# Performance work log

Hardware: AMD Instinct MI355X
Metric: run time of the kernel (lower is better)

Reference implementation:

```python
import jax, jax.numpy as jnp
import numpy as np
from jax import lax

NUM_HEADS = 4
NUM_GROUPS = 32
EPS = 1e-5


def group_norm(x, gamma, beta):
    # x: [b, c, t]
    b, c, t = x.shape
    xg = x.reshape(b, NUM_GROUPS, c // NUM_GROUPS, t)
    mu = jnp.mean(xg, axis=(2, 3), keepdims=True)
    var = jnp.var(xg, axis=(2, 3), keepdims=True)
    xg = (xg - mu) * lax.rsqrt(var + EPS)
    x = xg.reshape(b, c, t)
    return x * gamma[None, :, None] + beta[None, :, None]


def conv1d_same(x, w, b):
    # x: [b, c_in, t], w: [c_out, c_in, k] -> TF-style SAME padding, stride 1
    k = w.shape[-1]
    left = (k - 1) // 2
    right = (k - 1) - left
    y = lax.conv_general_dilated(x, w, window_strides=(1,),
                                 padding=[(left, right)],
                                 dimension_numbers=('NCH', 'OIH', 'NCH'))
    return y + b[None, :, None]


def qkv_attention(qkv):
    # qkv: [b*heads, 3*ch, t]
    ch = qkv.shape[1] // 3
    q, k, v = jnp.split(qkv, 3, axis=1)
    scale = float(ch) ** -0.25  # 1/sqrt(sqrt(ch)) applied to both q and k
    w = jnp.einsum('bct,bcs->bts', q * scale, k * scale)
    w = jax.nn.softmax(w.astype(jnp.float32), axis=-1).astype(qkv.dtype)
    return jnp.einsum('bts,bcs->bct', w, v)


def setup_inputs() -> dict:
    key = jax.random.key(0)
    ks = jax.random.split(key, 5)
    B, C, H, W = 4, 512, 64, 64
    x = jax.random.normal(ks[0], (B, C, H, W), dtype=jnp.float32)
    gn_gamma = jnp.ones((C,), dtype=jnp.float32)
    gn_beta = jnp.zeros((C,), dtype=jnp.float32)
    qkv_w = jax.random.normal(ks[1], (3 * C, C, C // 16), dtype=jnp.float32) * 0.02
    qkv_b = jax.random.normal(ks[2], (3 * C,), dtype=jnp.float32) * 0.02
    proj_w = jax.random.normal(ks[3], (C, C, 5), dtype=jnp.float32) * 0.02
    proj_b = jax.random.normal(ks[4], (C,), dtype=jnp.float32) * 0.02
    return {"x": x, "gn_gamma": gn_gamma, "gn_beta": gn_beta,
            "qkv_w": qkv_w, "qkv_b": qkv_b, "proj_w": proj_w, "proj_b": proj_b}


def reference(x, gn_gamma, gn_beta, qkv_w, qkv_b, proj_w, proj_b):
    b, c = x.shape[0], x.shape[1]
    spatial = x.shape[2:]
    t = int(np.prod(spatial))
    xf = x.reshape(b, c, t)
    qkv = conv1d_same(group_norm(xf, gn_gamma, gn_beta), qkv_w, qkv_b)  # [b, 3c, t]
    qkv = qkv.reshape(b * NUM_HEADS, -1, t)
    h = qkv_attention(qkv)               # [b*heads, c//heads, t]
    h = h.reshape(b, -1, t)              # [b, c, t]
    h = conv1d_same(h, proj_w, proj_b)
    return (xf + h).reshape(b, c, *spatial)
```

## Files before the change

kernel.cpp:

```cpp
#include <hip/hip_runtime.h>
#include <hip/hip_bf16.h>
#include <math.h>

typedef __attribute__((ext_vector_type(8))) __bf16 bf16x8;
typedef __attribute__((ext_vector_type(4))) float  f32x4;

__device__ __forceinline__ unsigned short f2bf(float f) {
    union { float f; unsigned int u; } x; x.f = f;
    unsigned int r = x.u + 0x7fffu + ((x.u >> 16) & 1u);
    return (unsigned short)(r >> 16);
}

__device__ __forceinline__ void gl_lds16(const unsigned short* g, unsigned short* l) {
    auto gp = (const unsigned int __attribute__((address_space(1)))*)((const void*)g);
    auto lp = (unsigned int __attribute__((address_space(3)))*)(unsigned int)(unsigned long long)((void*)l);
    __builtin_amdgcn_global_load_lds(gp, lp, 16, 0, 0);
}

#define B_   4
#define C_   512
#define T_   4096
#define NH   4
#define DH   128

__global__ __launch_bounds__(256) void cvt_wqkv(const float* __restrict__ w, unsigned short* __restrict__ o) {
    __shared__ unsigned short l[512 * 33];
    int co = blockIdx.x;
    const float* src = w + (size_t)co * 16384;
    for (int j = 0; j < 64; j++) {
        int i = threadIdx.x + j * 256;
        l[(i >> 5) * 33 + (i & 31)] = f2bf(src[i]);
    }
    __syncthreads();
    unsigned short* dst = o + (size_t)co * 16384;
    for (int j = 0; j < 64; j++) {
        int i = threadIdx.x + j * 256;
        int dk = i >> 9, ci = i & 511;
        dst[i] = l[ci * 33 + dk];
    }
}

__global__ __launch_bounds__(256) void cvt_wproj(const float* __restrict__ w, unsigned short* __restrict__ o) {
    __shared__ unsigned short l[512 * 6];
    int co = blockIdx.x;
    const float* src = w + (size_t)co * 2560;
    for (int j = 0; j < 10; j++) {
        int i = threadIdx.x + j * 256;
        int ci = i / 5, dk = i - ci * 5;
        l[ci * 6 + dk] = f2bf(src[i]);
    }
    __syncthreads();
    unsigned short* dst = o + (size_t)co * 2560;
    for (int j = 0; j < 10; j++) {
        int i = threadIdx.x + j * 256;
        int dk = i >> 9, ci = i & 511;
        dst[i] = l[ci * 6 + dk];
    }
}

__global__ __launch_bounds__(1024) void groupnorm(const float* __restrict__ x,
                                                  const float* __restrict__ gamma,
                                                  const float* __restrict__ beta,
                                                  unsigned short* __restrict__ gnT) {
    int g = blockIdx.x, b = blockIdx.y;
    int tid = threadIdx.x;
    const float* base = x + ((size_t)b * C_ + g * 16) * T_;
    const float4* b4 = (const float4*)base;
    float4 v[16];
    float s = 0.f, s2 = 0.f;
#pragma unroll
    for (int j = 0; j < 16; j++) {
        float4 w = b4[tid + j * 1024];
        v[j] = w;
        s  += w.x + w.y + w.z + w.w;
        s2 += w.x * w.x + w.y * w.y + w.z * w.z + w.w * w.w;
    }
    for (int off = 32; off; off >>= 1) { s += __shfl_down(s, off, 64); s2 += __shfl_down(s2, off, 64); }
    __shared__ float red[34];
    int wid = tid >> 6, lane = tid & 63;
    if (lane == 0) { red[wid] = s; red[16 + wid] = s2; }
    __syncthreads();
    if (tid == 0) {
        float ts = 0.f, ts2 = 0.f;
        for (int i = 0; i < 16; i++) { ts += red[i]; ts2 += red[16 + i]; }
        float mu = ts / 65536.f;
        float var = ts2 / 65536.f - mu * mu;
        red[32] = mu; red[33] = rsqrtf(var + 1e-5f);
    }
    __syncthreads();
    float mu = red[32], inv = red[33];
    float gm[16], bt[16];
#pragma unroll
    for (int cc = 0; cc < 16; cc++) { gm[cc] = gamma[g * 16 + cc] * inv; bt[cc] = beta[g * 16 + cc]; }
#pragma unroll
    for (int e = 0; e < 4; e++) {
        int t = tid * 4 + e;
        unsigned short outv[16];
#pragma unroll
        for (int cc = 0; cc < 16; cc++) {
            float xv = (e == 0) ? v[cc].x : (e == 1) ? v[cc].y : (e == 2) ? v[cc].z : v[cc].w;
            outv[cc] = f2bf((xv - mu) * gm[cc] + bt[cc]);
        }
        unsigned short* dst = gnT + ((size_t)b * T_ + t) * C_ + g * 16;
        *(uint4*)dst       = *(uint4*)outv;
        *(uint4*)(dst + 8) = *(uint4*)(outv + 8);
    }
}

__global__ __launch_bounds__(256, 2) void gemm_qkv(const unsigned short* __restrict__ gnT,
                                                   const unsigned short* __restrict__ wq,
                                                   const float* __restrict__ bias,
                                                   unsigned short* __restrict__ qT,
                                                   unsigned short* __restrict__ kT,
                                                   unsigned short* __restrict__ vv) {
    int b = blockIdx.x & 3, nblk = blockIdx.x >> 2, mblk = blockIdx.y;
    int m0 = mblk * 128, t0 = nblk * 256;
    __shared__ unsigned short As[2][128 * 64];
    __shared__ unsigned short Bsl[288 * 64];
    int tid = threadIdx.x, lane = tid & 63, wave = tid >> 6;
    int quad = lane >> 4, l16 = lane & 15;
    int wm = wave & 1, wn = wave >> 1;

    const unsigned short* gb = gnT + (size_t)b * T_ * C_;
    int srow = tid >> 3, spc = tid & 7;

    int fo[2];
    fo[0] = ((quad ^ (l16 & 7)) << 3);
    fo[1] = (((4 + quad) ^ (l16 & 7)) << 3);
    int rowb = wn * 128 + l16;

    f32x4 acc[4][8];
    f32x4 z4 = {0.f, 0.f, 0.f, 0.f};
#pragma unroll
    for (int mt = 0; mt < 4; mt++)
#pragma unroll
        for (int nt = 0; nt < 8; nt++) acc[mt][nt] = z4;

    bool isF = (nblk == 0), isL = (nblk == 15);

    for (int cc = 0; cc < 8; cc++) {
#pragma unroll
        for (int i = 0; i < 9; i++) {
            int row = i * 32 + srow;
            int p = spc ^ (row & 7);
            gl_lds16(gb + (size_t)(t0 - 15 + row) * 512 + cc * 64 + p * 8,
                     Bsl + (i * 256 + wave * 64) * 8);
        }
#pragma unroll
        for (int i = 0; i < 4; i++) {
            int row = i * 32 + srow;
            int p = spc ^ (row & 7);
            gl_lds16(wq + (size_t)(m0 + row) * 16384 + cc * 64 + p * 8,
                     As[0] + (i * 256 + wave * 64) * 8);
        }
        __syncthreads();
        if (isF) {
            if (tid < 15 * 8) *(uint4*)&Bsl[(tid >> 3) * 64 + (tid & 7) * 8] = make_uint4(0, 0, 0, 0);
            __syncthreads();
        }
        if (isL) {
            if (tid < 17 * 8) *(uint4*)&Bsl[(271 + (tid >> 3)) * 64 + (tid & 7) * 8] = make_uint4(0, 0, 0, 0);
            __syncthreads();
        }
        for (int dk = 0; dk < 32; dk++) {
            int cur = dk & 1;
            if (dk != 31) {
#pragma unroll
                for (int i = 0; i < 4; i++) {
                    int row = i * 32 + srow;
                    int p = spc ^ (row & 7);
                    gl_lds16(wq + (size_t)(m0 + row) * 16384 + (dk + 1) * 512 + cc * 64 + p * 8,
                             As[cur ^ 1] + (i * 256 + wave * 64) * 8);
                }
            }
            int rd = rowb + dk;
            int pb0 = ((quad ^ (rd & 7)) << 3);
            int pb1 = (((4 + quad) ^ (rd & 7)) << 3);
#pragma unroll
            for (int kk = 0; kk < 2; kk++) {
                int pbk = kk ? pb1 : pb0;
                bf16x8 af[4], bfr[8];
#pragma unroll
                for (int mt = 0; mt < 4; mt++)
                    af[mt] = *(const bf16x8*)&As[cur][(wm * 64 + mt * 16 + l16) * 64 + fo[kk]];
#pragma unroll
                for (int nt = 0; nt < 8; nt++)
                    bfr[nt] = *(const bf16x8*)&Bsl[(rd + nt * 16) * 64 + pbk];
#pragma unroll
                for (int mt = 0; mt < 4; mt++)
#pragma unroll
                    for (int nt = 0; nt < 8; nt++)
                        acc[mt][nt] = __builtin_amdgcn_mfma_f32_16x16x32_bf16(af[mt], bfr[nt], acc[mt][nt], 0, 0, 0);
            }
            __syncthreads();
        }
    }
#pragma unroll
    for (int mt = 0; mt < 4; mt++) {
        int cobase = m0 + wm * 64 + mt * 16 + quad * 4;
        int h = cobase / 384;
        int local = cobase - h * 384;
        int bh = b * NH + h;
#pragma unroll
        for (int nt = 0; nt < 8; nt++) {
            int t = t0 + wn * 128 + nt * 16 + l16;
            f32x4 a = acc[mt][nt];
            unsigned short r4[4];
            for (int r = 0; r < 4; r++) r4[r] = f2bf(a[r] + bias[cobase + r]);
            if (local < 128) {
                unsigned short* dst = qT + ((size_t)bh * T_ + t) * DH + local;
                *(uint2*)dst = *(uint2*)r4;
            } else if (local < 256) {
                unsigned short* dst = kT + ((size_t)bh * T_ + t) * DH + (local - 128);
                *(uint2*)dst = *(uint2*)r4;
            } else {
                unsigned short* dst = vv + ((size_t)bh * DH + (local - 256)) * T_ + t;
                for (int r = 0; r < 4; r++) dst[(size_t)r * T_] = r4[r];
            }
        }
    }
}

__global__ __launch_bounds__(256, 2) void attn(const unsigned short* __restrict__ qT,
                                               const unsigned short* __restrict__ kT,
                                               const unsigned short* __restrict__ vv,
                                               unsigned short* __restrict__ hT) {
    int q0 = blockIdx.x * 128, bh = blockIdx.y;
    int b = bh >> 2, h = bh & 3;
    __shared__ unsigned short Ks[64 * 128];
    __shared__ unsigned short Vs[128 * 64];
    __shared__ unsigned short Ps[128 * 72];
    int tid = threadIdx.x, lane = tid & 63, wave = tid >> 6, quad = lane >> 4, l16 = lane & 15;

    bf16x8 bq[2][4];
#pragma unroll
    for (int u = 0; u < 2; u++) {
        const unsigned short* qrow = qT + ((size_t)bh * T_ + q0 + wave * 32 + u * 16 + l16) * DH + quad * 8;
#pragma unroll
        for (int kk = 0; kk < 4; kk++) bq[u][kk] = *(const bf16x8*)(qrow + kk * 32);
    }

    const unsigned short* kbase = kT + (size_t)bh * T_ * DH;
    const unsigned short* vbase = vv + (size_t)bh * DH * T_;
    int krow_in = lane >> 4, kp = lane & 15;
    int vrow_in = lane >> 3, vp = lane & 7;

    float m_i[2] = {-1e30f, -1e30f}, l_i[2] = {0.f, 0.f};
    f32x4 z4 = {0.f, 0.f, 0.f, 0.f};
    f32x4 o[2][8];
#pragma unroll
    for (int u = 0; u < 2; u++)
#pragma unroll
        for (int nt = 0; nt < 8; nt++) o[u][nt] = z4;
    const float scale2 = 0.08838834764831845f;

    for (int ts0 = 0; ts0 < T_; ts0 += 64) {
        __syncthreads();
#pragma unroll
        for (int i = 0; i < 4; i++) {
            int row = (wave * 4 + i) * 4 + krow_in;
            gl_lds16(kbase + ((size_t)(ts0 + row)) * DH + (((kp ^ (row & 7)) << 3)),
                     Ks + (wave * 4 + i) * 512);
        }
#pragma unroll
        for (int i = 0; i < 4; i++) {
            int row = (wave * 4 + i) * 8 + vrow_in;
            gl_lds16(vbase + (size_t)row * T_ + ts0 + (((vp ^ (row & 7)) << 3)),
                     Vs + (wave * 4 + i) * 512);
        }
        __syncthreads();

        f32x4 s[2][4];
#pragma unroll
        for (int u = 0; u < 2; u++)
#pragma unroll
            for (int mt = 0; mt < 4; mt++) s[u][mt] = z4;
#pragma unroll
        for (int kk = 0; kk < 4; kk++) {
            int pb = (((kk * 4 + quad) ^ (l16 & 7)) << 3);
#pragma unroll
            for (int mt = 0; mt < 4; mt++) {
                bf16x8 ak = *(const bf16x8*)&Ks[(mt * 16 + l16) * 128 + pb];
                s[0][mt] = __builtin_amdgcn_mfma_f32_16x16x32_bf16(ak, bq[0][kk], s[0][mt], 0, 0, 0);
                s[1][mt] = __builtin_amdgcn_mfma_f32_16x16x32_bf16(ak, bq[1][kk], s[1][mt], 0, 0, 0);
            }
        }
#pragma unroll
        for (int u = 0; u < 2; u++) {
            float mx = -1e30f;
#pragma unroll
            for (int mt = 0; mt < 4; mt++) {
                s[u][mt] *= scale2;
                mx = fmaxf(mx, fmaxf(fmaxf(s[u][mt][0], s[u][mt][1]), fmaxf(s[u][mt][2], s[u][mt][3])));
            }
            mx = fmaxf(mx, __shfl_xor(mx, 16, 64));
            mx = fmaxf(mx, __shfl_xor(mx, 32, 64));
            float mnew = fmaxf(m_i[u], mx);
            float alpha = __expf(m_i[u] - mnew);
            float rs = 0.f;
#pragma unroll
            for (int mt = 0; mt < 4; mt++) {
#pragma unroll
                for (int r = 0; r < 4; r++) { float p = __expf(s[u][mt][r] - mnew); s[u][mt][r] = p; rs += p; }
            }
            rs += __shfl_xor(rs, 16, 64);
            rs += __shfl_xor(rs, 32, 64);
            m_i[u] = mnew;
            l_i[u] = l_i[u] * alpha + rs;
#pragma unroll
            for (int mt = 0; mt < 4; mt++) {
                unsigned short t4[4];
#pragma unroll
                for (int r = 0; r < 4; r++) t4[r] = f2bf(s[u][mt][r]);
                *(uint2*)&Ps[(wave * 32 + u * 16 + l16) * 72 + mt * 16 + quad * 4] = *(uint2*)t4;
            }
            float a0 = __shfl(alpha, quad * 4 + 0, 64);
            float a1 = __shfl(alpha, quad * 4 + 1, 64);
            float a2 = __shfl(alpha, quad * 4 + 2, 64);
            float a3 = __shfl(alpha, quad * 4 + 3, 64);
            f32x4 av = {a0, a1, a2, a3};
#pragma unroll
            for (int nt = 0; nt < 8; nt++) o[u][nt] *= av;
        }
#pragma unroll
        for (int kk = 0; kk < 2; kk++) {
            int pb = (((kk * 4 + quad) ^ (l16 & 7)) << 3);
            bf16x8 ap0 = *(const bf16x8*)&Ps[(wave * 32 + l16) * 72 + kk * 32 + quad * 8];
            bf16x8 ap1 = *(const bf16x8*)&Ps[(wave * 32 + 16 + l16) * 72 + kk * 32 + quad * 8];
#pragma unroll
            for (int nt = 0; nt < 8; nt++) {
                bf16x8 bv = *(const bf16x8*)&Vs[(nt * 16 + l16) * 64 + pb];
                o[0][nt] = __builtin_amdgcn_mfma_f32_16x16x32_bf16(ap0, bv, o[0][nt], 0, 0, 0);
                o[1][nt] = __builtin_amdgcn_mfma_f32_16x16x32_bf16(ap1, bv, o[1][nt], 0, 0, 0);
            }
        }
    }
#pragma unroll
    for (int u = 0; u < 2; u++) {
        float i0 = 1.f / __shfl(l_i[u], quad * 4 + 0, 64);
        float i1 = 1.f / __shfl(l_i[u], quad * 4 + 1, 64);
        float i2 = 1.f / __shfl(l_i[u], quad * 4 + 2, 64);
        float i3 = 1.f / __shfl(l_i[u], quad * 4 + 3, 64);
        f32x4 iv = {i0, i1, i2, i3};
#pragma unroll
        for (int r = 0; r < 4; r++) {
            int t = q0 + wave * 32 + u * 16 + quad * 4 + r;
            unsigned short* dst = hT + ((size_t)b * T_ + t) * C_ + h * DH;
#pragma unroll
            for (int nt = 0; nt < 8; nt++) dst[nt * 16 + l16] = f2bf(o[u][nt][r] * iv[r]);
        }
    }
}

__global__ __launch_bounds__(256, 3) void gemm_proj(const unsigned short* __restrict__ hT,
                                                    const unsigned short* __restrict__ wp,
                                                    const float* __restrict__ bias,
                                                    const float* __restrict__ x,
                                                    float* __restrict__ out) {
    int nblk = blockIdx.x, mblk = blockIdx.y, b = blockIdx.z;
    int m0 = mblk * 128, t0 = nblk * 128;
    __shared__ unsigned short As[128 * 64], Bs[128 * 64];
    int tid = threadIdx.x, lane = tid & 63, wave = tid >> 6;
    int quad = lane >> 4, l16 = lane & 15;
    int wm = wave & 1, wn = wave >> 1;

    int srow8 = lane >> 3;
    int scb = (lane & 7) ^ srow8;
    const unsigned short* hb = hT + (size_t)b * T_ * C_;
    const unsigned short* ap[4]; const unsigned short* bp[4];
    unsigned short *la[4], *lb[4];
#pragma unroll
    for (int i = 0; i < 4; i++) {
        int g = wave * 4 + i;
        int row = g * 8 + srow8;
        ap[i] = wp + (size_t)(m0 + row) * 2560 + scb * 8;
        bp[i] = hb + ((size_t)(t0 - 2 + row)) * 512 + scb * 8;
        la[i] = As + g * 512;
        lb[i] = Bs + g * 512;
    }
    const unsigned short* pAr[2]; const unsigned short* pBr[2];
#pragma unroll
    for (int kk = 0; kk < 2; kk++) {
        pAr[kk] = As + (wm * 64 + l16) * 64 + (((kk * 4 + quad) ^ (l16 & 7)) << 3);
        pBr[kk] = Bs + (wn * 64 + l16) * 64 + (((kk * 4 + quad) ^ (l16 & 7)) << 3);
    }
    f32x4 acc[4][4];
    f32x4 z4 = {0.f, 0.f, 0.f, 0.f};
#pragma unroll
    for (int mt = 0; mt < 4; mt++)
#pragma unroll
        for (int nt = 0; nt < 4; nt++) acc[mt][nt] = z4;

    bool isF = (nblk == 0), isL = (nblk == 31);
    for (int s = 0; s < 40; s++) {
        __syncthreads();
#pragma unroll
        for (int i = 0; i < 4; i++) { gl_lds16(ap[i], la[i]); ap[i] += 64; }
#pragma unroll
        for (int i = 0; i < 4; i++) { gl_lds16(bp[i], lb[i]); bp[i] += 64; }
        __syncthreads();
        int dk = s >> 3;
        if (isF && dk < 2) {
            int nz = 2 - dk, r = tid >> 3;
            if (r < nz) *(uint4*)&Bs[(r << 6) + ((tid & 7) << 3)] = make_uint4(0, 0, 0, 0);
            __syncthreads();
        }
        if (isL && dk > 2) {
            int nb = dk - 2, rr = tid >> 3;
            if (rr < nb) *(uint4*)&Bs[((128 - nb + rr) << 6) + ((tid & 7) << 3)] = make_uint4(0, 0, 0, 0);
            __syncthreads();
        }
#pragma unroll
        for (int kk = 0; kk < 2; kk++) {
            bf16x8 af[4], bfr[4];
#pragma unroll
            for (int mt = 0; mt < 4; mt++) af[mt]  = *(const bf16x8*)(pAr[kk] + mt * 1024);
#pragma unroll
            for (int nt = 0; nt < 4; nt++) bfr[nt] = *(const bf16x8*)(pBr[kk] + nt * 1024);
#pragma unroll
            for (int mt = 0; mt < 4; mt++)
#pragma unroll
                for (int nt = 0; nt < 4; nt++)
                    acc[mt][nt] = __builtin_amdgcn_mfma_f32_16x16x32_bf16(af[mt], bfr[nt], acc[mt][nt], 0, 0, 0);
        }
    }
#pragma unroll
    for (int mt = 0; mt < 4; mt++) {
        int cobase = m0 + wm * 64 + mt * 16 + quad * 4;
#pragma unroll
        for (int nt = 0; nt < 4; nt++) {
            int t = t0 + wn * 64 + nt * 16 + l16;
            for (int r = 0; r < 4; r++) {
                int co = cobase + r;
                size_t idx = ((size_t)(b * C_ + co)) * T_ + t;
                out[idx] = acc[mt][nt][r] + bias[co] + x[idx];
            }
        }
    }
}

extern "C" void kernel_launch(void* const* d_in, const int* in_sizes, int n_in,
                              void* d_out, int out_size, void* d_ws, size_t ws_size,
                              hipStream_t stream) {
    const float* x      = (const float*)d_in[0];
    const float* gamma  = (const float*)d_in[1];
    const float* beta   = (const float*)d_in[2];
    const float* qkv_w  = (const float*)d_in[3];
    const float* qkv_b  = (const float*)d_in[4];
    const float* proj_w = (const float*)d_in[5];
    const float* proj_b = (const float*)d_in[6];
    float* out = (float*)d_out;
    char* ws = (char*)d_ws;

    unsigned short* wqkvT  = (unsigned short*)(ws);
    unsigned short* wprojT = (unsigned short*)(ws + 50331648);
    unsigned short* gnT    = (unsigned short*)(ws + 52953088);
    unsigned short* qTb    = (unsigned short*)(ws + 69730304);
    unsigned short* kTb    = (unsigned short*)(ws + 86507520);
    unsigned short* vb     = (unsigned short*)(ws + 103284736);
    unsigned short* hT     = gnT;

    hipLaunchKernelGGL(cvt_wqkv,  dim3(1536),     dim3(256),  0, stream, qkv_w, wqkvT);
    hipLaunchKernelGGL(cvt_wproj, dim3(512),      dim3(256),  0, stream, proj_w, wprojT);
    hipLaunchKernelGGL(groupnorm, dim3(32, 4),    dim3(1024), 0, stream, x, gamma, beta, gnT);
    hipLaunchKernelGGL(gemm_qkv,  dim3(64, 12),   dim3(256),  0, stream, gnT, wqkvT, qkv_b, qTb, kTb, vb);
    hipLaunchKernelGGL(attn,      dim3(32, 16),   dim3(256),  0, stream, qTb, kTb, vb, hT);
    hipLaunchKernelGGL(gemm_proj, dim3(32, 4, 4), dim3(256),  0, stream, hT, wprojT, proj_b, x, out);
}
```

Before: 1.016 ms.

## Prepack QKV weights in MFMA fragment order and double-buffer GEMM and attention loads

The weight conversion kernel now writes QKV weights in a layout matching the MFMA A-fragment lane order. The QKV GEMM then loads A fragments straight from global memory into registers, prefetched one step ahead, instead of staging them through LDS with a barrier per tap. The GEMM's B tile is double-buffered across channel chunks. The attention kernel double-buffers its K/V tiles and replaces the padded P buffer with an XOR-swizzled one. The aim is fewer barriers and more overlap of loads with MFMA. The cost is more LDS and registers, and the conversion kernel now launches only 96 blocks.

```diff
diff --git a/kernel.cpp b/kernel.cpp
--- a/kernel.cpp
+++ b/kernel.cpp
@@ -24,19 +24,32 @@
 #define DH   128
 
 __global__ __launch_bounds__(256) void cvt_wqkv(const float* __restrict__ w, unsigned short* __restrict__ o) {
-    __shared__ unsigned short l[512 * 33];
-    int co = blockIdx.x;
-    const float* src = w + (size_t)co * 16384;
-    for (int j = 0; j < 64; j++) {
-        int i = threadIdx.x + j * 256;
-        l[(i >> 5) * 33 + (i & 31)] = f2bf(src[i]);
-    }
-    __syncthreads();
-    unsigned short* dst = o + (size_t)co * 16384;
-    for (int j = 0; j < 64; j++) {
-        int i = threadIdx.x + j * 256;
-        int dk = i >> 9, ci = i & 511;
-        dst[i] = l[ci * 33 + dk];
+    __shared__ unsigned short l[16 * 2312];
+    int g = blockIdx.x;
+    int tid = threadIdx.x;
+    for (int cc = 0; cc < 8; cc++) {
+        __syncthreads();
+        for (int it = 0; it < 32; it++) {
+            int idx = tid + it * 256;
+            int co = idx >> 9;
+            int rem = (idx & 511) * 4;
+            float4 v = *(const float4*)(w + (size_t)(g * 16 + co) * 16384 + cc * 2048 + rem);
+            int ci_l = rem >> 5, dk = rem & 31;
+            unsigned short* dst = &l[co * 2312 + dk * 72 + ci_l];
+            dst[0]   = f2bf(v.x);
+            dst[72]  = f2bf(v.y);
+            dst[144] = f2bf(v.z);
+            dst[216] = f2bf(v.w);
+        }
+        __syncthreads();
+        for (int it = 0; it < 16; it++) {
+            int oidx = tid + it * 256;
+            int lane = oidx & 63;
+            int kk = (oidx >> 6) & 1, dk = oidx >> 7;
+            int co = lane & 15, quad = lane >> 4;
+            uint4 val = *(const uint4*)&l[co * 2312 + dk * 72 + kk * 32 + quad * 8];
+            *(uint4*)&o[((((size_t)g * 256 + cc * 32 + dk) * 2 + kk) * 64 + lane) * 8] = val;
+        }
     }
 }
 
@@ -108,15 +121,14 @@
 }
 
 __global__ __launch_bounds__(256, 2) void gemm_qkv(const unsigned short* __restrict__ gnT,
-                                                   const unsigned short* __restrict__ wq,
+                                                   const unsigned short* __restrict__ wf,
                                                    const float* __restrict__ bias,
                                                    unsigned short* __restrict__ qT,
                                                    unsigned short* __restrict__ kT,
                                                    unsigned short* __restrict__ vv) {
     int b = blockIdx.x & 3, nblk = blockIdx.x >> 2, mblk = blockIdx.y;
     int m0 = mblk * 128, t0 = nblk * 256;
-    __shared__ unsigned short As[2][128 * 64];
-    __shared__ unsigned short Bsl[288 * 64];
+    __shared__ unsigned short Bsl[2][288 * 64];
     int tid = threadIdx.x, lane = tid & 63, wave = tid >> 6;
     int quad = lane >> 4, l16 = lane & 15;
     int wm = wave & 1, wn = wave >> 1;
@@ -124,11 +136,12 @@
     const unsigned short* gb = gnT + (size_t)b * T_ * C_;
     int srow = tid >> 3, spc = tid & 7;
 
-    int fo[2];
-    fo[0] = ((quad ^ (l16 & 7)) << 3);
-    fo[1] = (((4 + quad) ^ (l16 & 7)) << 3);
+    const unsigned short* apb[4];
+#pragma unroll
+    for (int mt = 0; mt < 4; mt++)
+        apb[mt] = wf + ((size_t)(mblk * 8 + wm * 4 + mt) * 512) * 512 + lane * 8;
+
     int rowb = wn * 128 + l16;
-
     f32x4 acc[4][8];
     f32x4 z4 = {0.f, 0.f, 0.f, 0.f};
 #pragma unroll
@@ -138,61 +151,63 @@
 
     bool isF = (nblk == 0), isL = (nblk == 15);
 
+#pragma unroll
+    for (int i = 0; i < 9; i++) {
+        int row = i * 32 + srow;
+        gl_lds16(gb + (size_t)(t0 - 15 + row) * 512 + ((spc ^ (row & 7)) << 3),
+                 Bsl[0] + (i * 256 + wave * 64) * 8);
+    }
+    __syncthreads();
+    if (isF) { if (tid < 120) *(uint4*)&Bsl[0][(tid >> 3) * 64 + ((tid & 7) << 3)] = make_uint4(0, 0, 0, 0); }
+    if (isL) { if (tid < 136) *(uint4*)&Bsl[0][(271 + (tid >> 3)) * 64 + ((tid & 7) << 3)] = make_uint4(0, 0, 0, 0); }
+    if (isF || isL) __syncthreads();
+
+    bf16x8 af[2][2][4];
+#pragma unroll
+    for (int kk = 0; kk < 2; kk++)
+#pragma unroll
+        for (int mt = 0; mt < 4; mt++) af[0][kk][mt] = *(const bf16x8*)(apb[mt] + kk * 512);
+
     for (int cc = 0; cc < 8; cc++) {
-#pragma unroll
-        for (int i = 0; i < 9; i++) {
-            int row = i * 32 + srow;
-            int p = spc ^ (row & 7);
-            gl_lds16(gb + (size_t)(t0 - 15 + row) * 512 + cc * 64 + p * 8,
-                     Bsl + (i * 256 + wave * 64) * 8);
-        }
-#pragma unroll
-        for (int i = 0; i < 4; i++) {
-            int row = i * 32 + srow;
-            int p = spc ^ (row & 7);
-            gl_lds16(wq + (size_t)(m0 + row) * 16384 + cc * 64 + p * 8,
-                     As[0] + (i * 256 + wave * 64) * 8);
+        int cur = cc & 1;
+        if (cc < 7) {
+#pragma unroll
+            for (int i = 0; i < 9; i++) {
+                int row = i * 32 + srow;
+                gl_lds16(gb + (size_t)(t0 - 15 + row) * 512 + (cc + 1) * 64 + ((spc ^ (row & 7)) << 3),
+                         Bsl[cur ^ 1] + (i * 256 + wave * 64) * 8);
+            }
+        }
+        for (int dk = 0; dk < 32; dk++) {
+            int p = dk & 1;
+            if (!(cc == 7 && dk == 31)) {
+                int ns = (dk < 31) ? (cc * 32 + dk + 1) : ((cc + 1) * 32);
+#pragma unroll
+                for (int kk = 0; kk < 2; kk++)
+#pragma unroll
+                    for (int mt = 0; mt < 4; mt++)
+                        af[p ^ 1][kk][mt] = *(const bf16x8*)(apb[mt] + (ns * 2 + kk) * 512);
+            }
+            int rd = rowb + dk;
+#pragma unroll
+            for (int kk = 0; kk < 2; kk++) {
+                int pbk = (((kk * 4 + quad) ^ (rd & 7)) << 3);
+                bf16x8 bfr[8];
+#pragma unroll
+                for (int nt = 0; nt < 8; nt++)
+                    bfr[nt] = *(const bf16x8*)&Bsl[cur][(rd + nt * 16) * 64 + pbk];
+#pragma unroll
+                for (int mt = 0; mt < 4; mt++)
+#pragma unroll
+                    for (int nt = 0; nt < 8; nt++)
+                        acc[mt][nt] = __builtin_amdgcn_mfma_f32_16x16x32_bf16(af[p][kk][mt], bfr[nt], acc[mt][nt], 0, 0, 0);
+            }
         }
         __syncthreads();
-        if (isF) {
-            if (tid < 15 * 8) *(uint4*)&Bsl[(tid >> 3) * 64 + (tid & 7) * 8] = make_uint4(0, 0, 0, 0);
-            __syncthreads();
-        }
-        if (isL) {
-            if (tid < 17 * 8) *(uint4*)&Bsl[(271 + (tid >> 3)) * 64 + (tid & 7) * 8] = make_uint4(0, 0, 0, 0);
-            __syncthreads();
-        }
-        for (int dk = 0; dk < 32; dk++) {
-            int cur = dk & 1;
-            if (dk != 31) {
-#pragma unroll
-                for (int i = 0; i < 4; i++) {
-                    int row = i * 32 + srow;
-                    int p = spc ^ (row & 7);
-                    gl_lds16(wq + (size_t)(m0 + row) * 16384 + (dk + 1) * 512 + cc * 64 + p * 8,
-                             As[cur ^ 1] + (i * 256 + wave * 64) * 8);
-                }
-            }
-            int rd = rowb + dk;
-            int pb0 = ((quad ^ (rd & 7)) << 3);
-            int pb1 = (((4 + quad) ^ (rd & 7)) << 3);
-#pragma unroll
-            for (int kk = 0; kk < 2; kk++) {
-                int pbk = kk ? pb1 : pb0;
-                bf16x8 af[4], bfr[8];
-#pragma unroll
-                for (int mt = 0; mt < 4; mt++)
-                    af[mt] = *(const bf16x8*)&As[cur][(wm * 64 + mt * 16 + l16) * 64 + fo[kk]];
-#pragma unroll
-                for (int nt = 0; nt < 8; nt++)
-                    bfr[nt] = *(const bf16x8*)&Bsl[(rd + nt * 16) * 64 + pbk];
-#pragma unroll
-                for (int mt = 0; mt < 4; mt++)
-#pragma unroll
-                    for (int nt = 0; nt < 8; nt++)
-                        acc[mt][nt] = __builtin_amdgcn_mfma_f32_16x16x32_bf16(af[mt], bfr[nt], acc[mt][nt], 0, 0, 0);
-            }
-            __syncthreads();
+        if (cc < 7) {
+            if (isF) { if (tid < 120) *(uint4*)&Bsl[cur ^ 1][(tid >> 3) * 64 + ((tid & 7) << 3)] = make_uint4(0, 0, 0, 0); }
+            if (isL) { if (tid < 136) *(uint4*)&Bsl[cur ^ 1][(271 + (tid >> 3)) * 64 + ((tid & 7) << 3)] = make_uint4(0, 0, 0, 0); }
+            if (isF || isL) __syncthreads();
         }
     }
 #pragma unroll
@@ -227,9 +242,9 @@
                                                unsigned short* __restrict__ hT) {
     int q0 = blockIdx.x * 128, bh = blockIdx.y;
     int b = bh >> 2, h = bh & 3;
-    __shared__ unsigned short Ks[64 * 128];
-    __shared__ unsigned short Vs[128 * 64];
-    __shared__ unsigned short Ps[128 * 72];
+    __shared__ unsigned short Ks[2][64 * 128];
+    __shared__ unsigned short Vs[2][128 * 64];
+    __shared__ unsigned short Ps[128 * 64];
     int tid = threadIdx.x, lane = tid & 63, wave = tid >> 6, quad = lane >> 4, l16 = lane & 15;
 
     bf16x8 bq[2][4];
@@ -254,21 +269,34 @@
         for (int nt = 0; nt < 8; nt++) o[u][nt] = z4;
     const float scale2 = 0.08838834764831845f;
 
+#pragma unroll
+    for (int i = 0; i < 4; i++) {
+        int row = (wave * 4 + i) * 4 + krow_in;
+        gl_lds16(kbase + (size_t)row * DH + ((kp ^ (row & 7)) << 3), Ks[0] + (wave * 4 + i) * 512);
+    }
+#pragma unroll
+    for (int i = 0; i < 4; i++) {
+        int row = (wave * 4 + i) * 8 + vrow_in;
+        gl_lds16(vbase + (size_t)row * T_ + ((vp ^ (row & 7)) << 3), Vs[0] + (wave * 4 + i) * 512);
+    }
+    __syncthreads();
+
     for (int ts0 = 0; ts0 < T_; ts0 += 64) {
-        __syncthreads();
-#pragma unroll
-        for (int i = 0; i < 4; i++) {
-            int row = (wave * 4 + i) * 4 + krow_in;
-            gl_lds16(kbase + ((size_t)(ts0 + row)) * DH + (((kp ^ (row & 7)) << 3)),
-                     Ks + (wave * 4 + i) * 512);
-        }
-#pragma unroll
-        for (int i = 0; i < 4; i++) {
-            int row = (wave * 4 + i) * 8 + vrow_in;
-            gl_lds16(vbase + (size_t)row * T_ + ts0 + (((vp ^ (row & 7)) << 3)),
-                     Vs + (wave * 4 + i) * 512);
-        }
-        __syncthreads();
+        int cur = (ts0 >> 6) & 1;
+        if (ts0 + 64 < T_) {
+#pragma unroll
+            for (int i = 0; i < 4; i++) {
+                int row = (wave * 4 + i) * 4 + krow_in;
+                gl_lds16(kbase + (size_t)(ts0 + 64 + row) * DH + ((kp ^ (row & 7)) << 3),
+                         Ks[cur ^ 1] + (wave * 4 + i) * 512);
+            }
+#pragma unroll
+            for (int i = 0; i < 4; i++) {
+                int row = (wave * 4 + i) * 8 + vrow_in;
+                gl_lds16(vbase + (size_t)row * T_ + ts0 + 64 + ((vp ^ (row & 7)) << 3),
+                         Vs[cur ^ 1] + (wave * 4 + i) * 512);
+            }
+        }
 
         f32x4 s[2][4];
 #pragma unroll
@@ -280,13 +308,14 @@
             int pb = (((kk * 4 + quad) ^ (l16 & 7)) << 3);
 #pragma unroll
             for (int mt = 0; mt < 4; mt++) {
-                bf16x8 ak = *(const bf16x8*)&Ks[(mt * 16 + l16) * 128 + pb];
+                bf16x8 ak = *(const bf16x8*)&Ks[cur][(mt * 16 + l16) * 128 + pb];
                 s[0][mt] = __builtin_amdgcn_mfma_f32_16x16x32_bf16(ak, bq[0][kk], s[0][mt], 0, 0, 0);
                 s[1][mt] = __builtin_amdgcn_mfma_f32_16x16x32_bf16(ak, bq[1][kk], s[1][mt], 0, 0, 0);
             }
         }
 #pragma unroll
         for (int u = 0; u < 2; u++) {
+            int prow = wave * 32 + u * 16 + l16;
             float mx = -1e30f;
 #pragma unroll
             for (int mt = 0; mt < 4; mt++) {
@@ -312,7 +341,8 @@
                 unsigned short t4[4];
 #pragma unroll
                 for (int r = 0; r < 4; r++) t4[r] = f2bf(s[u][mt][r]);
-                *(uint2*)&Ps[(wave * 32 + u * 16 + l16) * 72 + mt * 16 + quad * 4] = *(uint2*)t4;
+                int blk = (mt * 2 + (quad >> 1)) ^ (prow & 7);
+                *(uint2*)&Ps[prow * 64 + (blk << 3) + ((quad & 1) << 2)] = *(uint2*)t4;
             }
             float a0 = __shfl(alpha, quad * 4 + 0, 64);
             float a1 = __shfl(alpha, quad * 4 + 1, 64);
@@ -325,15 +355,17 @@
 #pragma unroll
         for (int kk = 0; kk < 2; kk++) {
             int pb = (((kk * 4 + quad) ^ (l16 & 7)) << 3);
-            bf16x8 ap0 = *(const bf16x8*)&Ps[(wave * 32 + l16) * 72 + kk * 32 + quad * 8];
-            bf16x8 ap1 = *(const bf16x8*)&Ps[(wave * 32 + 16 + l16) * 72 + kk * 32 + quad * 8];
+            int prow0 = wave * 32 + l16, prow1 = wave * 32 + 16 + l16;
+            bf16x8 ap0 = *(const bf16x8*)&Ps[prow0 * 64 + ((((kk * 4 + quad) ^ (prow0 & 7))) << 3)];
+            bf16x8 ap1 = *(const bf16x8*)&Ps[prow1 * 64 + ((((kk * 4 + quad) ^ (prow1 & 7))) << 3)];
 #pragma unroll
             for (int nt = 0; nt < 8; nt++) {
-                bf16x8 bv = *(const bf16x8*)&Vs[(nt * 16 + l16) * 64 + pb];
+                bf16x8 bv = *(const bf16x8*)&Vs[cur][(nt * 16 + l16) * 64 + pb];
                 o[0][nt] = __builtin_amdgcn_mfma_f32_16x16x32_bf16(ap0, bv, o[0][nt], 0, 0, 0);
                 o[1][nt] = __builtin_amdgcn_mfma_f32_16x16x32_bf16(ap1, bv, o[1][nt], 0, 0, 0);
             }
         }
+        __syncthreads();
     }
 #pragma unroll
     for (int u = 0; u < 2; u++) {
@@ -452,7 +484,7 @@
     float* out = (float*)d_out;
     char* ws = (char*)d_ws;
 
-    unsigned short* wqkvT  = (unsigned short*)(ws);
+    unsigned short* wqkvF  = (unsigned short*)(ws);
     unsigned short* wprojT = (unsigned short*)(ws + 50331648);
     unsigned short* gnT    = (unsigned short*)(ws + 52953088);
     unsigned short* qTb    = (unsigned short*)(ws + 69730304);
@@ -460,10 +492,10 @@
     unsigned short* vb     = (unsigned short*)(ws + 103284736);
     unsigned short* hT     = gnT;
 
-    hipLaunchKernelGGL(cvt_wqkv,  dim3(1536),     dim3(256),  0, stream, qkv_w, wqkvT);
+    hipLaunchKernelGGL(cvt_wqkv,  dim3(96),       dim3(256),  0, stream, qkv_w, wqkvF);
     hipLaunchKernelGGL(cvt_wproj, dim3(512),      dim3(256),  0, stream, proj_w, wprojT);
     hipLaunchKernelGGL(groupnorm, dim3(32, 4),    dim3(1024), 0, stream, x, gamma, beta, gnT);
-    hipLaunchKernelGGL(gemm_qkv,  dim3(64, 12),   dim3(256),  0, stream, gnT, wqkvT, qkv_b, qTb, kTb, vb);
+    hipLaunchKernelGGL(gemm_qkv,  dim3(64, 12),   dim3(256),  0, stream, gnT, wqkvF, qkv_b, qTb, kTb, vb);
     hipLaunchKernelGGL(attn,      dim3(32, 16),   dim3(256),  0, stream, qTb, kTb, vb, hT);
     hipLaunchKernelGGL(gemm_proj, dim3(32, 4, 4), dim3(256),  0, stream, hT, wprojT, proj_b, x, out);
 }
```

Measured after the change: 2.345 ms. +130.8%, slower.
